# Kernel optimization log

Hardware: AMD Instinct MI355X
Metric: run time of the kernel (lower is better)

Reference implementation:

```python
import jax, jax.numpy as jnp
import numpy as np

EMBED_DIM = 300
HIDDEN_DIM = 500
NUM_LAYERS = 2
NUM_CLASSES = 20
VOCAB = 100000
SEQ_LEN = 2048


def setup_inputs() -> dict:
    key = jax.random.key(0)
    ks = jax.random.split(key, 12)
    s = 1.0 / np.sqrt(HIDDEN_DIM)
    inp = {
        "sequence": jax.random.randint(ks[0], (SEQ_LEN,), 0, VOCAB),
        "emb": jax.random.normal(ks[1], (VOCAB, EMBED_DIM), jnp.float32),
        # layer 0: input dim 300
        "W_ih0": jax.random.normal(ks[2], (4 * HIDDEN_DIM, EMBED_DIM), jnp.float32) * s,
        "W_hh0": jax.random.normal(ks[3], (4 * HIDDEN_DIM, HIDDEN_DIM), jnp.float32) * s,
        "b_ih0": jax.random.normal(ks[4], (4 * HIDDEN_DIM,), jnp.float32) * s,
        "b_hh0": jax.random.normal(ks[5], (4 * HIDDEN_DIM,), jnp.float32) * s,
        # layer 1: input dim 500
        "W_ih1": jax.random.normal(ks[6], (4 * HIDDEN_DIM, HIDDEN_DIM), jnp.float32) * s,
        "W_hh1": jax.random.normal(ks[7], (4 * HIDDEN_DIM, HIDDEN_DIM), jnp.float32) * s,
        "b_ih1": jax.random.normal(ks[8], (4 * HIDDEN_DIM,), jnp.float32) * s,
        "b_hh1": jax.random.normal(ks[9], (4 * HIDDEN_DIM,), jnp.float32) * s,
        "fc_W": jax.random.normal(ks[10], (NUM_CLASSES, HIDDEN_DIM), jnp.float32) * s,
        "fc_b": jax.random.normal(ks[11], (NUM_CLASSES,), jnp.float32) * s,
    }
    return inp


def _lstm_layer(x_seq, W_ih, W_hh, b_ih, b_hh):
    """Scan a single LSTM layer over the full sequence. x_seq: [T, D_in]."""
    H = W_hh.shape[1]
    # precompute input projections for all timesteps: [T, 4H]
    x_proj = x_seq @ W_ih.T + b_ih + b_hh

    def step(carry, xp):
        h, c = carry
        gates = xp + h @ W_hh.T  # [4H], PyTorch gate order i, f, g, o
        i, f, g, o = jnp.split(gates, 4)
        i = jax.nn.sigmoid(i)
        f = jax.nn.sigmoid(f)
        g = jnp.tanh(g)
        o = jax.nn.sigmoid(o)
        c = f * c + i * g
        h = o * jnp.tanh(c)
        return (h, c), h

    init = (jnp.zeros((H,), x_seq.dtype), jnp.zeros((H,), x_seq.dtype))
    _, hs = jax.lax.scan(step, init, x_proj)
    return hs  # [T, H]


def reference(sequence, emb, W_ih0, W_hh0, b_ih0, b_hh0, W_ih1, W_hh1, b_ih1, b_hh1, fc_W, fc_b):
    x = emb[sequence]                                   # [T, 300]
    h0 = _lstm_layer(x, W_ih0, W_hh0, b_ih0, b_hh0)     # [T, 500]
    h1 = _lstm_layer(h0, W_ih1, W_hh1, b_ih1, b_hh1)    # [T, 500]
    out = h1[-1] @ fc_W.T + fc_b                        # last timestep -> [num_classes]
    return out.reshape(1, -1)
```

## Files before the change

kernel.cpp:

```cpp
#include <hip/hip_runtime.h>

#define T_STEPS 2048
#define H       500
#define E       300
#define HP      512
#define XPT     2048
#define NCLS    20
#define NB0     125
#define NB1     125
#define BIAS2   2.0f

typedef float v4f __attribute__((ext_vector_type(4)));

__device__ __forceinline__ float sigm_(float x){ return 1.0f/(1.0f+__expf(-x)); }
__device__ __forceinline__ float tanh_(float x){ return 2.0f/(1.0f+__expf(-2.0f*x)) - 1.0f; }

__device__ __forceinline__ v4f v4z() { v4f r; r.x=0.f; r.y=0.f; r.z=0.f; r.w=0.f; return r; }
__device__ __forceinline__ v4f v4sub(v4f v, float s){ v4f r; r.x=v.x-s; r.y=v.y-s; r.z=v.z-s; r.w=v.w-s; return r; }
__device__ __forceinline__ bool nz4(v4f v){ return v.x!=0.f && v.y!=0.f && v.z!=0.f && v.w!=0.f; }
__device__ __forceinline__ float dot4(v4f w, v4f x){ return w.x*x.x + w.y*x.y + w.z*x.z + w.w*x.w; }

__device__ __forceinline__ void poll2(const float* p0, const float* p1, v4f& a, v4f& b) {
    asm volatile("global_load_dwordx4 %0, %2, off sc0 sc1\n\t"
                 "global_load_dwordx4 %1, %3, off sc0 sc1\n\t"
                 "s_waitcnt vmcnt(0)"
                 : "=&v"(a), "=&v"(b)
                 : "v"(p0), "v"(p1));
}
__device__ __forceinline__ void store1_cc(float* p, float v) {
    asm volatile("global_store_dword %0, %1, off sc0 sc1" :: "v"(p), "v"(v));
}

__global__ __launch_bounds__(256) void lstm_init(float* hs) {
    int i = blockIdx.x*256 + threadIdx.x;
    const int NH4 = (T_STEPS+1)*HP/4;
    v4f b2; b2.x=BIAS2; b2.y=BIAS2; b2.z=BIAS2; b2.w=BIAS2;
    bool seed = (i < H/4) || (i >= NH4 && i < NH4 + H/4);
    ((v4f*)hs)[i] = seed ? b2 : v4z();
}

__global__ __launch_bounds__(256) void xproj_kernel(
    const int* __restrict__ seq, const float* __restrict__ emb,
    const float* __restrict__ Wih0, const float* __restrict__ bih0,
    const float* __restrict__ bhh0, float* __restrict__ xp)
{
    __shared__ float xe[16][308];
    const int tid = threadIdx.x;
    const int t0 = blockIdx.x * 16;
    for (int i = tid; i < 16*76; i += 256) {
        int tt = i / 76, c4 = (i - tt*76) * 4;
        v4f val = v4z();
        if (c4 < E) val = *(const v4f*)&emb[(size_t)seq[t0+tt]*E + c4];
        *(v4f*)&xe[tt][c4] = val;
    }
    __syncthreads();
    const int rg = tid >> 4, tl = tid & 15;
    for (int k = 0; k < 125; ++k) {
        int row = k*16 + rg;
        const float* wr = Wih0 + (size_t)row*E;
        float acc = bih0[row] + bhh0[row];
        #pragma unroll 5
        for (int c = 0; c < 75; ++c)
            acc += dot4(*(const v4f*)(wr + 4*c), *(const v4f*)&xe[tl][4*c]);
        xp[(size_t)row*XPT + t0 + tl] = acc;
    }
}

__device__ __forceinline__ float reduce16(float* acc, int lane) {
    float v8[8];
    {
        const bool b = lane & 1;
        #pragma unroll
        for (int i = 0; i < 8; ++i) {
            float keep = b ? acc[8+i] : acc[i];
            float send = b ? acc[i]   : acc[8+i];
            v8[i] = keep + __shfl_xor(send, 1, 64);
        }
    }
    float v4a[4];
    {
        const bool b = lane & 2;
        #pragma unroll
        for (int i = 0; i < 4; ++i) {
            float keep = b ? v8[4+i] : v8[i];
            float send = b ? v8[i]   : v8[4+i];
            v4a[i] = keep + __shfl_xor(send, 2, 64);
        }
    }
    float v2a[2];
    {
        const bool b = lane & 4;
        #pragma unroll
        for (int i = 0; i < 2; ++i) {
            float keep = b ? v4a[2+i] : v4a[i];
            float send = b ? v4a[i]   : v4a[2+i];
            v2a[i] = keep + __shfl_xor(send, 4, 64);
        }
    }
    float v1;
    {
        const bool b = lane & 8;
        float keep = b ? v2a[1] : v2a[0];
        float send = b ? v2a[0] : v2a[1];
        v1 = keep + __shfl_xor(send, 8, 64);
    }
    v1 += __shfl_xor(v1, 16, 64);
    v1 += __shfl_xor(v1, 32, 64);
    return v1;
}

__device__ __forceinline__ float gates_combine(float x, int b2, int b3, float& cs) {
    const bool isG = (b2 == 1 && b3 == 0);
    float a = 1.f/(1.f + __expf(isG ? -2.f*x : -x));
    float act = isG ? 2.f*a - 1.f : a;
    float t1 = __shfl_xor(act, 4, 64);
    float t2 = __shfl_xor(act, 8, 64);
    float t3 = __shfl_xor(act, 12, 64);
    float gi = b2 ? (b3 ? t3 : t1) : (b3 ? t2 : act);
    float gf = b2 ? (b3 ? t1 : t3) : (b3 ? act : t2);
    float gg = b2 ? (b3 ? t2 : act) : (b3 ? t3 : t1);
    float go = b2 ? (b3 ? act : t2) : (b3 ? t1 : t3);
    cs = gf*cs + gi*gg;
    return go * tanh_(cs);
}

__launch_bounds__(128, 1)
__global__ void lstm_main(
    const float* __restrict__ Whh0,
    const float* __restrict__ Wih1, const float* __restrict__ Whh1,
    const float* __restrict__ bih1, const float* __restrict__ bhh1,
    const float* __restrict__ fcW, const float* __restrict__ fcb,
    float* __restrict__ out,
    const float* __restrict__ xp, float* h0s, float* h1s)
{
    __shared__ float part[2][64];
    const int blk  = blockIdx.x;
    const int wid  = threadIdx.x >> 6;
    const int lane = threadIdx.x & 63;
    const int c0 = 8*lane;
    const bool need0 = (c0 + 4 <= H);
    const bool need1 = (c0 + 8 <= H);
    const int b0 = lane&1, b1=(lane>>1)&1, b2=(lane>>2)&1, b3=(lane>>3)&1;
    const int unit = 2*b0 + b1;
    const int gate = 2*b2 + b3;

    if (blk < NB0) {
        if (wid == 1) return;
        const int u0 = 4*blk;
        v4f w[16][2];
        #pragma unroll
        for (int r = 0; r < 16; ++r) {
            const int R_ = (r&3)*H + u0 + (r>>2);
            const float* wh = Whh0 + (size_t)R_*H;
            w[r][0] = need0 ? *(const v4f*)(wh + c0)     : v4z();
            w[r][1] = need1 ? *(const v4f*)(wh + c0 + 4) : v4z();
        }
        const float* xpp = xp + (size_t)(gate*H + u0 + unit)*XPT;
        float cs = 0.f;

        for (int t = 1; t <= T_STEPS; ++t) {
            float xpv = xpp[t-1];
            const float* hp = h0s + (size_t)(t-1)*HP;
            v4f A = v4z(), B = v4z();
            bool ok = !(need0 || need1);
            while (!__all(ok)) {
                if (!ok) {
                    poll2(hp + c0, hp + c0 + 4, A, B);
                    ok = (!need0 || nz4(A)) && (!need1 || nz4(B));
                }
            }
            v4f i0 = v4sub(A, BIAS2), i1 = v4sub(B, BIAS2);
            float acc[16];
            #pragma unroll
            for (int r = 0; r < 16; ++r)
                acc[r] = dot4(w[r][0], i0) + dot4(w[r][1], i1);
            float v = reduce16(acc, lane);
            float hval = gates_combine(v + xpv, b2, b3, cs);
            if ((lane & 60) == 0)
                store1_cc(h0s + (size_t)t*HP + u0 + unit, hval + BIAS2);
        }
    } else {
        const int g  = blk - NB0;
        const int u0 = 4*g;
        if (wid == 0) {
            v4f w[16][2];
            float bsum;
            {
                const int R_ = gate*H + u0 + unit;
                bsum = bih1[R_] + bhh1[R_];
            }
            #pragma unroll
            for (int r = 0; r < 16; ++r) {
                const int R_ = (r&3)*H + u0 + (r>>2);
                const float* wi = Wih1 + (size_t)R_*H;
                w[r][0] = need0 ? *(const v4f*)(wi + c0)     : v4z();
                w[r][1] = need1 ? *(const v4f*)(wi + c0 + 4) : v4z();
            }
            float cs = 0.f;
            for (int t = 1; t <= T_STEPS; ++t) {
                const float* hp = h0s + (size_t)t*HP;
                v4f A = v4z(), B = v4z();
                bool ok = !(need0 || need1);
                while (!__all(ok)) {
                    if (!ok) {
                        poll2(hp + c0, hp + c0 + 4, A, B);
                        ok = (!need0 || nz4(A)) && (!need1 || nz4(B));
                    }
                }
                v4f i0 = v4sub(A, BIAS2), i1 = v4sub(B, BIAS2);
                float acc[16];
                #pragma unroll
                for (int r = 0; r < 16; ++r)
                    acc[r] = dot4(w[r][0], i0) + dot4(w[r][1], i1);
                float v = reduce16(acc, lane);
                __syncthreads();
                v += part[t&1][lane];
                float hval = gates_combine(v + bsum, b2, b3, cs);
                if ((lane & 60) == 0)
                    store1_cc(h1s + (size_t)t*HP + u0 + unit, hval + BIAS2);
            }
            if (g == 0) {
                const float* hT = h1s + (size_t)T_STEPS*HP;
                v4f A = v4z(), B = v4z();
                bool ok = !(need0 || need1);
                while (!__all(ok)) {
                    if (!ok) {
                        poll2(hT + c0, hT + c0 + 4, A, B);
                        ok = (!need0 || nz4(A)) && (!need1 || nz4(B));
                    }
                }
                v4f h0v = need0 ? v4sub(A, BIAS2) : v4z();
                v4f h1v = need1 ? v4sub(B, BIAS2) : v4z();
                #pragma unroll 4
                for (int r = 0; r < NCLS; ++r) {
                    const float* wr = fcW + (size_t)r*H;
                    v4f wa = need0 ? *(const v4f*)(wr + c0)     : v4z();
                    v4f wb = need1 ? *(const v4f*)(wr + c0 + 4) : v4z();
                    float a = dot4(wa, h0v) + dot4(wb, h1v);
                    #pragma unroll
                    for (int m = 32; m >= 1; m >>= 1) a += __shfl_xor(a, m, 64);
                    if (lane == 0) out[r] = a + fcb[r];
                }
            }
        } else {
            v4f w[16][2];
            #pragma unroll
            for (int r = 0; r < 16; ++r) {
                const int R_ = (r&3)*H + u0 + (r>>2);
                const float* wh = Whh1 + (size_t)R_*H;
                w[r][0] = need0 ? *(const v4f*)(wh + c0)     : v4z();
                w[r][1] = need1 ? *(const v4f*)(wh + c0 + 4) : v4z();
            }
            for (int t = 1; t <= T_STEPS; ++t) {
                const float* hp = h1s + (size_t)(t-1)*HP;
                v4f A = v4z(), B = v4z();
                bool ok = !(need0 || need1);
                while (!__all(ok)) {
                    if (!ok) {
                        poll2(hp + c0, hp + c0 + 4, A, B);
                        ok = (!need0 || nz4(A)) && (!need1 || nz4(B));
                    }
                }
                v4f i0 = v4sub(A, BIAS2), i1 = v4sub(B, BIAS2);
                float acc[16];
                #pragma unroll
                for (int r = 0; r < 16; ++r)
                    acc[r] = dot4(w[r][0], i0) + dot4(w[r][1], i1);
                part[t&1][lane] = reduce16(acc, lane);
                __syncthreads();
            }
        }
    }
}

extern "C" void kernel_launch(void* const* d_in, const int* in_sizes, int n_in,
                              void* d_out, int out_size, void* d_ws, size_t ws_size,
                              hipStream_t stream)
{
    const int*   seq  = (const int*)d_in[0];
    const float* emb  = (const float*)d_in[1];
    const float* Whh0 = (const float*)d_in[3];
    const float* bih0 = (const float*)d_in[4];
    const float* bhh0 = (const float*)d_in[5];
    const float* Wih0 = (const float*)d_in[2];
    const float* Wih1 = (const float*)d_in[6];
    const float* Whh1 = (const float*)d_in[7];
    const float* bih1 = (const float*)d_in[8];
    const float* bhh1 = (const float*)d_in[9];
    const float* fcW  = (const float*)d_in[10];
    const float* fcb  = (const float*)d_in[11];
    float* out = (float*)d_out;

    float* h0s = (float*)d_ws;
    float* h1s = h0s + (size_t)(T_STEPS+1)*HP;
    float* xpj = h1s + (size_t)(T_STEPS+1)*HP;

    hipLaunchKernelGGL(lstm_init, dim3(2049), dim3(256), 0, stream, h0s);
    hipLaunchKernelGGL(xproj_kernel, dim3(T_STEPS/16), dim3(256), 0, stream,
                       seq, emb, Wih0, bih0, bhh0, xpj);
    hipLaunchKernelGGL(lstm_main, dim3(NB0 + NB1), dim3(128), 0, stream,
                       Whh0, Wih1, Whh1, bih1, bhh1, fcW, fcb, out, xpj, h0s, h1s);
}
```

Before: 5.896 ms.

## Restructure layer-1 into single-wave blocks with fused ih/hh dot and bias folding

Layer 1 previously used two waves per block (input and recurrent halves) joined by LDS and __syncthreads; now each single-wave block handles 2 units with both weight matrices in registers and polls h0[t] and h1[t-1] together, doubling the block count to 375. The BIAS2 subtraction on polled values is folded into a precomputed per-row offset (-2·rowsum). The column mapping changes to contiguous 4-float chunks at 4j and 256+4j, and inline asm pins keep weights resident in registers. This removes the intra-block barrier and the per-step subtracts, at the cost of more blocks spinning on global memory and a wider poll per step.

```diff
diff --git a/kernel.cpp b/kernel.cpp
--- a/kernel.cpp
+++ b/kernel.cpp
@@ -7,18 +7,19 @@
 #define XPT     2048
 #define NCLS    20
 #define NB0     125
-#define NB1     125
+#define NB1     250
 #define BIAS2   2.0f
 
 typedef float v4f __attribute__((ext_vector_type(4)));
 
-__device__ __forceinline__ float sigm_(float x){ return 1.0f/(1.0f+__expf(-x)); }
 __device__ __forceinline__ float tanh_(float x){ return 2.0f/(1.0f+__expf(-2.0f*x)) - 1.0f; }
-
 __device__ __forceinline__ v4f v4z() { v4f r; r.x=0.f; r.y=0.f; r.z=0.f; r.w=0.f; return r; }
 __device__ __forceinline__ v4f v4sub(v4f v, float s){ v4f r; r.x=v.x-s; r.y=v.y-s; r.z=v.z-s; r.w=v.w-s; return r; }
 __device__ __forceinline__ bool nz4(v4f v){ return v.x!=0.f && v.y!=0.f && v.z!=0.f && v.w!=0.f; }
 __device__ __forceinline__ float dot4(v4f w, v4f x){ return w.x*x.x + w.y*x.y + w.z*x.z + w.w*x.w; }
+__device__ __forceinline__ float sum4(v4f v){ return v.x+v.y+v.z+v.w; }
+
+#define PIN4(a,b,c,d) asm volatile("" : "+v"(a), "+v"(b), "+v"(c), "+v"(d))
 
 __device__ __forceinline__ void poll2(const float* p0, const float* p1, v4f& a, v4f& b) {
     asm volatile("global_load_dwordx4 %0, %2, off sc0 sc1\n\t"
@@ -26,6 +27,17 @@
                  "s_waitcnt vmcnt(0)"
                  : "=&v"(a), "=&v"(b)
                  : "v"(p0), "v"(p1));
+}
+__device__ __forceinline__ void poll4(const float* p0, const float* p1,
+                                      const float* p2, const float* p3,
+                                      v4f& a, v4f& b, v4f& c, v4f& d) {
+    asm volatile("global_load_dwordx4 %0, %4, off sc0 sc1\n\t"
+                 "global_load_dwordx4 %1, %5, off sc0 sc1\n\t"
+                 "global_load_dwordx4 %2, %6, off sc0 sc1\n\t"
+                 "global_load_dwordx4 %3, %7, off sc0 sc1\n\t"
+                 "s_waitcnt vmcnt(0)"
+                 : "=&v"(a), "=&v"(b), "=&v"(c), "=&v"(d)
+                 : "v"(p0), "v"(p1), "v"(p2), "v"(p3));
 }
 __device__ __forceinline__ void store1_cc(float* p, float v) {
     asm volatile("global_store_dword %0, %1, off sc0 sc1" :: "v"(p), "v"(v));
@@ -68,48 +80,63 @@
 
 __device__ __forceinline__ float reduce16(float* acc, int lane) {
     float v8[8];
-    {
-        const bool b = lane & 1;
-        #pragma unroll
-        for (int i = 0; i < 8; ++i) {
-            float keep = b ? acc[8+i] : acc[i];
-            float send = b ? acc[i]   : acc[8+i];
-            v8[i] = keep + __shfl_xor(send, 1, 64);
-        }
-    }
+    { const bool b = lane & 1;
+      #pragma unroll
+      for (int i = 0; i < 8; ++i) {
+        float keep = b ? acc[8+i] : acc[i];
+        float send = b ? acc[i]   : acc[8+i];
+        v8[i] = keep + __shfl_xor(send, 1, 64); } }
     float v4a[4];
-    {
-        const bool b = lane & 2;
-        #pragma unroll
-        for (int i = 0; i < 4; ++i) {
-            float keep = b ? v8[4+i] : v8[i];
-            float send = b ? v8[i]   : v8[4+i];
-            v4a[i] = keep + __shfl_xor(send, 2, 64);
-        }
-    }
+    { const bool b = lane & 2;
+      #pragma unroll
+      for (int i = 0; i < 4; ++i) {
+        float keep = b ? v8[4+i] : v8[i];
+        float send = b ? v8[i]   : v8[4+i];
+        v4a[i] = keep + __shfl_xor(send, 2, 64); } }
     float v2a[2];
-    {
-        const bool b = lane & 4;
-        #pragma unroll
-        for (int i = 0; i < 2; ++i) {
-            float keep = b ? v4a[2+i] : v4a[i];
-            float send = b ? v4a[i]   : v4a[2+i];
-            v2a[i] = keep + __shfl_xor(send, 4, 64);
-        }
-    }
+    { const bool b = lane & 4;
+      #pragma unroll
+      for (int i = 0; i < 2; ++i) {
+        float keep = b ? v4a[2+i] : v4a[i];
+        float send = b ? v4a[i]   : v4a[2+i];
+        v2a[i] = keep + __shfl_xor(send, 4, 64); } }
     float v1;
-    {
-        const bool b = lane & 8;
-        float keep = b ? v2a[1] : v2a[0];
-        float send = b ? v2a[0] : v2a[1];
-        v1 = keep + __shfl_xor(send, 8, 64);
-    }
+    { const bool b = lane & 8;
+      float keep = b ? v2a[1] : v2a[0];
+      float send = b ? v2a[0] : v2a[1];
+      v1 = keep + __shfl_xor(send, 8, 64); }
     v1 += __shfl_xor(v1, 16, 64);
     v1 += __shfl_xor(v1, 32, 64);
     return v1;
 }
 
-__device__ __forceinline__ float gates_combine(float x, int b2, int b3, float& cs) {
+__device__ __forceinline__ float reduce8(float* acc, int lane) {
+    float v4a[4];
+    { const bool b = lane & 1;
+      #pragma unroll
+      for (int i = 0; i < 4; ++i) {
+        float keep = b ? acc[4+i] : acc[i];
+        float send = b ? acc[i]   : acc[4+i];
+        v4a[i] = keep + __shfl_xor(send, 1, 64); } }
+    float v2a[2];
+    { const bool b = lane & 2;
+      #pragma unroll
+      for (int i = 0; i < 2; ++i) {
+        float keep = b ? v4a[2+i] : v4a[i];
+        float send = b ? v4a[i]   : v4a[2+i];
+        v2a[i] = keep + __shfl_xor(send, 2, 64); } }
+    float v1;
+    { const bool b = lane & 4;
+      float keep = b ? v2a[1] : v2a[0];
+      float send = b ? v2a[0] : v2a[1];
+      v1 = keep + __shfl_xor(send, 4, 64); }
+    v1 += __shfl_xor(v1, 8, 64);
+    v1 += __shfl_xor(v1, 16, 64);
+    v1 += __shfl_xor(v1, 32, 64);
+    return v1;
+}
+
+__device__ __forceinline__ float gates16(float x, int b2, int b3, float& cs) {
     const bool isG = (b2 == 1 && b3 == 0);
     float a = 1.f/(1.f + __expf(isG ? -2.f*x : -x));
     float act = isG ? 2.f*a - 1.f : a;
@@ -124,7 +151,22 @@
     return go * tanh_(cs);
 }
 
-__launch_bounds__(128, 1)
+__device__ __forceinline__ float gates8(float x, int g, float& cs) {
+    const bool isG = (g == 2);
+    float a = 1.f/(1.f + __expf(isG ? -2.f*x : -x));
+    float act = isG ? 2.f*a - 1.f : a;
+    float t1 = __shfl_xor(act, 4, 64);
+    float t2 = __shfl_xor(act, 2, 64);
+    float t3 = __shfl_xor(act, 6, 64);
+    float gi = (g==0)?act:(g==1)?t1:(g==2)?t2:t3;
+    float gf = (g==1)?act:(g==0)?t1:(g==3)?t2:t3;
+    float gg = (g==2)?act:(g==3)?t1:(g==0)?t2:t3;
+    float go = (g==3)?act:(g==2)?t1:(g==1)?t2:t3;
+    cs = gf*cs + gi*gg;
+    return go * tanh_(cs);
+}
+
+__launch_bounds__(64, 1)
 __global__ void lstm_main(
     const float* __restrict__ Whh0,
     const float* __restrict__ Wih1, const float* __restrict__ Whh1,
@@ -133,141 +175,121 @@
     float* __restrict__ out,
     const float* __restrict__ xp, float* h0s, float* h1s)
 {
-    __shared__ float part[2][64];
     const int blk  = blockIdx.x;
-    const int wid  = threadIdx.x >> 6;
-    const int lane = threadIdx.x & 63;
-    const int c0 = 8*lane;
-    const bool need0 = (c0 + 4 <= H);
-    const bool need1 = (c0 + 8 <= H);
-    const int b0 = lane&1, b1=(lane>>1)&1, b2=(lane>>2)&1, b3=(lane>>3)&1;
-    const int unit = 2*b0 + b1;
-    const int gate = 2*b2 + b3;
+    const int j    = (int)(threadIdx.x & 63);
+    const int b0 = j&1, b1=(j>>1)&1, b2=(j>>2)&1, b3=(j>>3)&1;
+    const int cA = 4*j, cB = 256 + 4*j;
+    const bool hasB = (cB + 4 <= H);
 
     if (blk < NB0) {
-        if (wid == 1) return;
         const int u0 = 4*blk;
-        v4f w[16][2];
+        const int unit = 2*b0 + b1, gate = 2*b2 + b3;
+        v4f w0[16], w1[16];
+        float rs[16];
         #pragma unroll
         for (int r = 0; r < 16; ++r) {
             const int R_ = (r&3)*H + u0 + (r>>2);
             const float* wh = Whh0 + (size_t)R_*H;
-            w[r][0] = need0 ? *(const v4f*)(wh + c0)     : v4z();
-            w[r][1] = need1 ? *(const v4f*)(wh + c0 + 4) : v4z();
-        }
+            w0[r] = *(const v4f*)(wh + cA);
+            w1[r] = hasB ? *(const v4f*)(wh + cB) : v4z();
+            rs[r] = sum4(w0[r]) + sum4(w1[r]);
+        }
+        const float off = -BIAS2 * reduce16(rs, j);
         const float* xpp = xp + (size_t)(gate*H + u0 + unit)*XPT;
         float cs = 0.f;
 
         for (int t = 1; t <= T_STEPS; ++t) {
+            PIN4(w0[0],w0[1],w0[2],w0[3]);   PIN4(w0[4],w0[5],w0[6],w0[7]);
+            PIN4(w0[8],w0[9],w0[10],w0[11]); PIN4(w0[12],w0[13],w0[14],w0[15]);
+            PIN4(w1[0],w1[1],w1[2],w1[3]);   PIN4(w1[4],w1[5],w1[6],w1[7]);
+            PIN4(w1[8],w1[9],w1[10],w1[11]); PIN4(w1[12],w1[13],w1[14],w1[15]);
             float xpv = xpp[t-1];
             const float* hp = h0s + (size_t)(t-1)*HP;
-            v4f A = v4z(), B = v4z();
-            bool ok = !(need0 || need1);
+            v4f A, B; bool ok = false;
             while (!__all(ok)) {
                 if (!ok) {
-                    poll2(hp + c0, hp + c0 + 4, A, B);
-                    ok = (!need0 || nz4(A)) && (!need1 || nz4(B));
+                    poll2(hp + cA, hp + cB, A, B);
+                    ok = nz4(A) && (!hasB || nz4(B));
                 }
             }
-            v4f i0 = v4sub(A, BIAS2), i1 = v4sub(B, BIAS2);
             float acc[16];
             #pragma unroll
             for (int r = 0; r < 16; ++r)
-                acc[r] = dot4(w[r][0], i0) + dot4(w[r][1], i1);
-            float v = reduce16(acc, lane);
-            float hval = gates_combine(v + xpv, b2, b3, cs);
-            if ((lane & 60) == 0)
+                acc[r] = dot4(w0[r], A) + dot4(w1[r], B);
+            float v = reduce16(acc, j);
+            float hval = gates16(v + xpv + off, b2, b3, cs);
+            if ((j & 60) == 0)
                 store1_cc(h0s + (size_t)t*HP + u0 + unit, hval + BIAS2);
         }
     } else {
-        const int g  = blk - NB0;
-        const int u0 = 4*g;
-        if (wid == 0) {
-            v4f w[16][2];
-            float bsum;
-            {
-                const int R_ = gate*H + u0 + unit;
-                bsum = bih1[R_] + bhh1[R_];
-            }
-            #pragma unroll
-            for (int r = 0; r < 16; ++r) {
-                const int R_ = (r&3)*H + u0 + (r>>2);
-                const float* wi = Wih1 + (size_t)R_*H;
-                w[r][0] = need0 ? *(const v4f*)(wi + c0)     : v4z();
-                w[r][1] = need1 ? *(const v4f*)(wi + c0 + 4) : v4z();
-            }
-            float cs = 0.f;
-            for (int t = 1; t <= T_STEPS; ++t) {
-                const float* hp = h0s + (size_t)t*HP;
-                v4f A = v4z(), B = v4z();
-                bool ok = !(need0 || need1);
-                while (!__all(ok)) {
-                    if (!ok) {
-                        poll2(hp + c0, hp + c0 + 4, A, B);
-                        ok = (!need0 || nz4(A)) && (!need1 || nz4(B));
-                    }
-                }
-                v4f i0 = v4sub(A, BIAS2), i1 = v4sub(B, BIAS2);
-                float acc[16];
-                #pragma unroll
-                for (int r = 0; r < 16; ++r)
-                    acc[r] = dot4(w[r][0], i0) + dot4(w[r][1], i1);
-                float v = reduce16(acc, lane);
-                __syncthreads();
-                v += part[t&1][lane];
-                float hval = gates_combine(v + bsum, b2, b3, cs);
-                if ((lane & 60) == 0)
-                    store1_cc(h1s + (size_t)t*HP + u0 + unit, hval + BIAS2);
-            }
-            if (g == 0) {
-                const float* hT = h1s + (size_t)T_STEPS*HP;
-                v4f A = v4z(), B = v4z();
-                bool ok = !(need0 || need1);
-                while (!__all(ok)) {
-                    if (!ok) {
-                        poll2(hT + c0, hT + c0 + 4, A, B);
-                        ok = (!need0 || nz4(A)) && (!need1 || nz4(B));
-                    }
-                }
-                v4f h0v = need0 ? v4sub(A, BIAS2) : v4z();
-                v4f h1v = need1 ? v4sub(B, BIAS2) : v4z();
-                #pragma unroll 4
-                for (int r = 0; r < NCLS; ++r) {
-                    const float* wr = fcW + (size_t)r*H;
-                    v4f wa = need0 ? *(const v4f*)(wr + c0)     : v4z();
-                    v4f wb = need1 ? *(const v4f*)(wr + c0 + 4) : v4z();
-                    float a = dot4(wa, h0v) + dot4(wb, h1v);
-                    #pragma unroll
-                    for (int m = 32; m >= 1; m >>= 1) a += __shfl_xor(a, m, 64);
-                    if (lane == 0) out[r] = a + fcb[r];
+        const int g1 = blk - NB0;
+        const int u0 = 2*g1;
+        const int unit = b0, gate = 2*b1 + b2;
+        v4f wa[8], wb[8], wc[8], wd[8];
+        float rs[8];
+        #pragma unroll
+        for (int r = 0; r < 8; ++r) {
+            const int R_ = (r&3)*H + u0 + (r>>2);
+            const float* wi = Wih1 + (size_t)R_*H;
+            const float* wh = Whh1 + (size_t)R_*H;
+            wa[r] = *(const v4f*)(wi + cA);
+            wb[r] = hasB ? *(const v4f*)(wi + cB) : v4z();
+            wc[r] = *(const v4f*)(wh + cA);
+            wd[r] = hasB ? *(const v4f*)(wh + cB) : v4z();
+            rs[r] = sum4(wa[r]) + sum4(wb[r]) + sum4(wc[r]) + sum4(wd[r]);
+        }
+        float off;
+        {
+            const int R_my = gate*H + u0 + unit;
+            off = bih1[R_my] + bhh1[R_my] - BIAS2 * reduce8(rs, j);
+        }
+        float cs = 0.f;
+
+        for (int t = 1; t <= T_STEPS; ++t) {
+            PIN4(wa[0],wa[1],wa[2],wa[3]); PIN4(wa[4],wa[5],wa[6],wa[7]);
+            PIN4(wb[0],wb[1],wb[2],wb[3]); PIN4(wb[4],wb[5],wb[6],wb[7]);
+            PIN4(wc[0],wc[1],wc[2],wc[3]); PIN4(wc[4],wc[5],wc[6],wc[7]);
+            PIN4(wd[0],wd[1],wd[2],wd[3]); PIN4(wd[4],wd[5],wd[6],wd[7]);
+            const float* pa = h0s + (size_t)t*HP;
+            const float* pb = h1s + (size_t)(t-1)*HP;
+            v4f A, B, C, D; bool ok = false;
+            while (!__all(ok)) {
+                if (!ok) {
+                    poll4(pa + cA, pa + cB, pb + cA, pb + cB, A, B, C, D);
+                    ok = nz4(A) && nz4(C) && (!hasB || (nz4(B) && nz4(D)));
                 }
             }
-        } else {
-            v4f w[16][2];
+            float acc[8];
             #pragma unroll
-            for (int r = 0; r < 16; ++r) {
-                const int R_ = (r&3)*H + u0 + (r>>2);
-                const float* wh = Whh1 + (size_t)R_*H;
-                w[r][0] = need0 ? *(const v4f*)(wh + c0)     : v4z();
-                w[r][1] = need1 ? *(const v4f*)(wh + c0 + 4) : v4z();
+            for (int r = 0; r < 8; ++r)
+                acc[r] = dot4(wa[r], A) + dot4(wb[r], B)
+                       + dot4(wc[r], C) + dot4(wd[r], D);
+            float v = reduce8(acc, j);
+            float hval = gates8(v + off, gate, cs);
+            if ((j & 62) == 0)
+                store1_cc(h1s + (size_t)t*HP + u0 + unit, hval + BIAS2);
+        }
+
+        if (g1 == 0) {
+            const float* hT = h1s + (size_t)T_STEPS*HP;
+            v4f A, B; bool ok = false;
+            while (!__all(ok)) {
+                if (!ok) {
+                    poll2(hT + cA, hT + cB, A, B);
+                    ok = nz4(A) && (!hasB || nz4(B));
+                }
             }
-            for (int t = 1; t <= T_STEPS; ++t) {
-                const float* hp = h1s + (size_t)(t-1)*HP;
-                v4f A = v4z(), B = v4z();
-                bool ok = !(need0 || need1);
-                while (!__all(ok)) {
-                    if (!ok) {
-                        poll2(hp + c0, hp + c0 + 4, A, B);
-                        ok = (!need0 || nz4(A)) && (!need1 || nz4(B));
-                    }
-                }
-                v4f i0 = v4sub(A, BIAS2), i1 = v4sub(B, BIAS2);
-                float acc[16];
+            v4f v0 = v4sub(A, BIAS2);
+            v4f v1 = hasB ? v4sub(B, BIAS2) : v4z();
+            #pragma unroll 4
+            for (int r = 0; r < NCLS; ++r) {
+                const float* wr = fcW + (size_t)r*H;
+                v4f fa = *(const v4f*)(wr + cA);
+                v4f fb = hasB ? *(const v4f*)(wr + cB) : v4z();
+                float a = dot4(fa, v0) + dot4(fb, v1);
                 #pragma unroll
-                for (int r = 0; r < 16; ++r)
-                    acc[r] = dot4(w[r][0], i0) + dot4(w[r][1], i1);
-                part[t&1][lane] = reduce16(acc, lane);
-                __syncthreads();
+                for (int m = 32; m >= 1; m >>= 1) a += __shfl_xor(a, m, 64);
+                if (j == 0) out[r] = a + fcb[r];
             }
         }
     }
@@ -279,10 +301,10 @@
 {
     const int*   seq  = (const int*)d_in[0];
     const float* emb  = (const float*)d_in[1];
+    const float* Wih0 = (const float*)d_in[2];
     const float* Whh0 = (const float*)d_in[3];
     const float* bih0 = (const float*)d_in[4];
     const float* bhh0 = (const float*)d_in[5];
-    const float* Wih0 = (const float*)d_in[2];
     const float* Wih1 = (const float*)d_in[6];
     const float* Whh1 = (const float*)d_in[7];
     const float* bih1 = (const float*)d_in[8];
@@ -298,6 +320,6 @@
     hipLaunchKernelGGL(lstm_init, dim3(2049), dim3(256), 0, stream, h0s);
     hipLaunchKernelGGL(xproj_kernel, dim3(T_STEPS/16), dim3(256), 0, stream,
                        seq, emb, Wih0, bih0, bhh0, xpj);
-    hipLaunchKernelGGL(lstm_main, dim3(NB0 + NB1), dim3(128), 0, stream,
+    hipLaunchKernelGGL(lstm_main, dim3(NB0 + NB1), dim3(64), 0, stream,
                        Whh0, Wih1, Whh1, bih1, bhh1, fcW, fcb, out, xpj, h0s, h1s);
 }
```

Result: slower. 7.683 ms (+30.3%).
